# Kernel optimization log

Measured on AMD Instinct MI355X. Metric: run time of the kernel, lower is better.

## Reference

```python
import jax, jax.numpy as jnp
import numpy as np

N = 100000      # nodes
E = 1600000     # directed edges
F_IN = 128      # node feature dim
H = 128         # hidden dim
C = 16          # classes


def setup_inputs() -> dict:
    key = jax.random.key(0)
    ks = jax.random.split(key, 8)
    s = 1.0 / np.sqrt(H)
    return {
        "x": jax.random.normal(ks[0], (N, F_IN), dtype=jnp.float32),
        "edge_index": jax.random.randint(ks[1], (2, E), 0, N, dtype=jnp.int32),
        "W1": jax.random.normal(ks[2], (F_IN, H), dtype=jnp.float32) * s,
        "b1": jnp.zeros((H,), jnp.float32),
        "W2": jax.random.normal(ks[3], (H, H), dtype=jnp.float32) * s,
        "b2": jnp.zeros((H,), jnp.float32),
        "W3": jax.random.normal(ks[4], (H, H), dtype=jnp.float32) * s,
        "b3": jnp.zeros((H,), jnp.float32),
        "Wfc": jax.random.normal(ks[5], (H, C), dtype=jnp.float32) * s,
        "bfc": jnp.zeros((C,), jnp.float32),
    }


def _gcn_conv(x, W, b, src, dst, norm):
    # x' = b + scatter_add over edges of norm * (x @ W)[src] into dst
    h = x @ W                                   # [N, H] dense GEMM
    msg = h[src] * norm[:, None]                # [E+N, H] gather + scale
    out = jax.ops.segment_sum(msg, dst, num_segments=N)  # scatter-add
    return out + b


def reference(x, edge_index, W1, b1, W2, b2, W3, b3, Wfc, bfc):
    loops = jnp.arange(N, dtype=edge_index.dtype)
    src = jnp.concatenate([edge_index[0], loops])   # [E+N] with self-loops
    dst = jnp.concatenate([edge_index[1], loops])
    # symmetric normalization deg^{-1/2}[src] * deg^{-1/2}[dst] (PyG default)
    deg = jax.ops.segment_sum(jnp.ones_like(dst, dtype=x.dtype), dst, num_segments=N)
    dinv = jax.lax.rsqrt(deg)                       # deg >= 1 due to self-loops
    norm = dinv[src] * dinv[dst]

    h = jax.nn.elu(_gcn_conv(x, W1, b1, src, dst, norm))   # dropout is identity in eval
    h = jax.nn.elu(_gcn_conv(h, W2, b2, src, dst, norm))
    h = jax.nn.elu(_gcn_conv(h, W3, b3, src, dst, norm))
    logits = h @ Wfc + bfc                                  # [N, C]
    return jax.nn.log_softmax(logits, axis=-1)
```

## Files before the change

### kernel.cpp

```cpp
#include <hip/hip_runtime.h>
#include <math.h>

#define HDIM 128
#define CDIM 16
#define CAP 48
#define ASTR 136
#define HSTR 132
#define NBINS 256
#define TILE 4096
#define NPBMAX 512
#define SORTCAP 7424

typedef unsigned short u16;
typedef unsigned int u32;
typedef __attribute__((ext_vector_type(8))) short short8;
typedef __attribute__((ext_vector_type(4))) float f32x4;
typedef __attribute__((ext_vector_type(2))) float f32x2;

__device__ inline u16 f2bf(float f) {
  u32 u = __float_as_uint(f);
  u += 0x7fffu + ((u >> 16) & 1u);
  return (u16)(u >> 16);
}
__device__ inline float bf_lo(u32 p) { return __uint_as_float(p << 16); }
__device__ inline float bf_hi(u32 p) { return __uint_as_float(p & 0xffff0000u); }
__device__ inline u32 pack2(float a, float b) {
  return (u32)f2bf(a) | ((u32)f2bf(b) << 16);
}
__device__ inline u32 cvtpk(float a, float b) {
  u32 r;
  asm("v_cvt_pk_bf16_f32 %0, %1, %2" : "=v"(r) : "v"(a), "v"(b));
  return r;
}
__device__ inline void acc_word(f32x2& acc, u32 w) {
  f32x2 x;
  x.x = __uint_as_float(w << 16);
  x.y = __uint_as_float(w & 0xffff0000u);
  asm("v_pk_add_f32 %0, %1, %2" : "=v"(acc) : "v"(x), "v"(acc));
}


__global__ __launch_bounds__(256) void bin_kernel(const int* __restrict__ ei,
                                                  int* __restrict__ cursor,
                                                  int2* __restrict__ bins,
                                                  int binCap, int E, int npb, int nbE,
                                                  int nbW, int N,
                                                  const float* __restrict__ W0,
                                                  const float* __restrict__ W1,
                                                  const float* __restrict__ W2,
                                                  u16* __restrict__ Wt,
                                                  u16* __restrict__ Arow,
                                                  u16* __restrict__ Brow) {
  int tid = threadIdx.x;
  if (blockIdx.x >= nbE) {
    if (blockIdx.x >= nbE + nbW) {
      if (tid < 16) ((uint4*)Arow)[tid] = make_uint4(0, 0, 0, 0);
      else if (tid < 32) ((uint4*)Brow)[tid - 16] = make_uint4(0, 0, 0, 0);
      return;
    }
    int t = (blockIdx.x - nbE) * 256 + tid;
    int which = t >> 14, idx = t & 16383;
    int n = idx >> 7, k = idx & 127;
    const float* W = which == 0 ? W0 : (which == 1 ? W1 : W2);
    Wt[(size_t)which * HDIM * HDIM + n * HDIM + k] = f2bf(W[k * HDIM + n]);
    return;
  }
  __shared__ int2 eds[TILE];
  __shared__ int base[NBINS], rank[NBINS], hist[NBINS];
  int t0 = blockIdx.x * TILE;
  int n = min(TILE, E - t0);
  for (int i = tid; i < NBINS; i += 256) { hist[i] = 0; rank[i] = 0; }
  __syncthreads();
  for (int i = tid; i < n; i += 256) {
    int s = ei[t0 + i];
    int d = ei[E + t0 + i];
    eds[i] = make_int2(d, s);
    atomicAdd(&hist[d / npb], 1);
  }
  __syncthreads();
  for (int i = tid; i < NBINS; i += 256) {
    int h = hist[i];
    base[i] = h ? atomicAdd(&cursor[i], h) : 0;
  }
  __syncthreads();
  for (int i = tid; i < n; i += 256) {
    int2 e = eds[i];
    int b = e.x / npb;
    int r = base[b] + atomicAdd(&rank[b], 1);
    if (r < binCap) bins[(size_t)b * binCap + r] = e;
  }
}

__global__ __launch_bounds__(256) void fill2_kernel(const int2* __restrict__ bins,
                                                    const int* __restrict__ cursor,
                                                    int binCap, int npb,
                                                    int* __restrict__ deg,
                                                    int* __restrict__ csr, int N) {
  __shared__ int hist[NPBMAX];
  __shared__ int base[NPBMAX + 1];
  __shared__ int sorted[SORTCAP];
  int b = blockIdx.x;
  int tid = threadIdx.x;
  int n0 = b * npb;
  int nn = min(npb, N - n0);
  if (nn <= 0) return;
  int cnt = min(min(cursor[b], binCap), SORTCAP);
  const int2* eb = bins + (size_t)b * binCap;
  for (int i = tid; i < nn; i += 256) hist[i] = 0;
  __syncthreads();
  for (int i = tid; i < cnt; i += 256) atomicAdd(&hist[eb[i].x - n0], 1);
  __syncthreads();
  if (tid == 0) {
    int s = 0;
    for (int i = 0; i < nn; ++i) { base[i] = s; s += hist[i]; }
    base[nn] = s;
  }
  __syncthreads();
  for (int i = tid; i < nn; i += 256) hist[i] = 0;
  __syncthreads();
  for (int i = tid; i < cnt; i += 256) {
    int2 e = eb[i];
    int loc = e.x - n0;
    sorted[base[loc] + atomicAdd(&hist[loc], 1)] = e.y;
  }
  __syncthreads();
  for (int i = tid; i < nn; i += 256) deg[n0 + i] = base[i + 1] - base[i];
  int total = nn * CAP;
  int* cout = csr + (size_t)n0 * CAP;
  for (int i = tid; i < total; i += 256) {
    int loc = (int)(((u32)(i >> 4) * 21846u) >> 16);
    int j = i - loc * CAP;
    int s0 = base[loc];
    int dc = min(base[loc + 1] - s0, CAP);
    cout[i] = j < dc ? sorted[s0 + j] : N;
  }
}


template <bool FP32IN>
__global__ __launch_bounds__(256) void gemm_k(const void* __restrict__ Xv,
                                              const u16* __restrict__ Wt,
                                              const int* __restrict__ deg,
                                              u16* __restrict__ G, int N) {
  __shared__ u16 As[64 * ASTR];
  __shared__ u16 Wsm[128 * ASTR];
  int tid = threadIdx.x;
  int row0 = blockIdx.x * 64;

  {
    int r = tid >> 2, c = tid & 3;
    int rg = row0 + r;
    if (rg >= N) rg = N - 1;
    uint4* dst = (uint4*)(As + r * ASTR + c * 32);
    if (FP32IN) {
      const float4* src = (const float4*)((const float*)Xv + (size_t)rg * HDIM + c * 32);
#pragma unroll
      for (int j = 0; j < 4; ++j) {
        float4 a = src[2 * j], b = src[2 * j + 1];
        uint4 o;
        o.x = pack2(a.x, a.y); o.y = pack2(a.z, a.w);
        o.z = pack2(b.x, b.y); o.w = pack2(b.z, b.w);
        dst[j] = o;
      }
    } else {
      const uint4* src = (const uint4*)((const u16*)Xv + (size_t)rg * HDIM + c * 32);
      dst[0] = src[0]; dst[1] = src[1]; dst[2] = src[2]; dst[3] = src[3];
    }
  }
  {
    int r = tid >> 1, h = tid & 1;
    const uint4* src = (const uint4*)(Wt + r * HDIM + h * 64);
    uint4* dst = (uint4*)(Wsm + r * ASTR + h * 64);
#pragma unroll
    for (int i = 0; i < 8; ++i) dst[i] = src[i];
  }
  __syncthreads();

  int w = tid >> 6;
  int l = tid & 63;
  int m = l & 15, q = l >> 4;

  f32x4 acc[8];
#pragma unroll
  for (int i = 0; i < 8; ++i) acc[i] = (f32x4){0.f, 0.f, 0.f, 0.f};

#pragma unroll
  for (int kc = 0; kc < 4; ++kc) {
    short8 af = *(const short8*)(As + (w * 16 + m) * ASTR + kc * 32 + q * 8);
#pragma unroll
    for (int nt = 0; nt < 8; ++nt) {
      short8 bfr = *(const short8*)(Wsm + (nt * 16 + m) * ASTR + kc * 32 + q * 8);
      acc[nt] = __builtin_amdgcn_mfma_f32_16x16x32_bf16(af, bfr, acc[nt], 0, 0, 0);
    }
  }
  __syncthreads();

  float dv[4];
#pragma unroll
  for (int r = 0; r < 4; ++r) {
    int rg = row0 + w * 16 + q * 4 + r;
    dv[r] = rsqrtf((float)(deg[rg < N ? rg : N - 1] + 1));
  }
#pragma unroll
  for (int nt = 0; nt < 8; ++nt)
#pragma unroll
    for (int r = 0; r < 4; ++r)
      As[(w * 16 + q * 4 + r) * ASTR + nt * 16 + m] = f2bf(acc[nt][r] * dv[r]);
  __syncthreads();

  {
    int r = tid >> 2, c = tid & 3;
    int rg = row0 + r;
    if (rg < N) {
      uint4* dst = (uint4*)(G + (size_t)rg * HDIM + c * 32);
      const uint4* src = (const uint4*)(As + r * ASTR + c * 32);
      dst[0] = src[0]; dst[1] = src[1]; dst[2] = src[2]; dst[3] = src[3];
    }
  }
}


__device__ inline void gather16(const u16* __restrict__ G, const int* __restrict__ deg,
                                const int* __restrict__ csr,
                                const float4* __restrict__ b4, int node, int l, float* v) {
  const char* Gb = (const char*)G;
  f32x2 p0, p1, p2, p3;
  {
    uint4 sr = *(const uint4*)(Gb + ((size_t)node << 8) + (l << 4));
    p0.x = bf_lo(sr.x); p0.y = bf_hi(sr.x);
    p1.x = bf_lo(sr.y); p1.y = bf_hi(sr.y);
    p2.x = bf_lo(sr.z); p2.y = bf_hi(sr.z);
    p3.x = bf_lo(sr.w); p3.y = bf_hi(sr.w);
  }
  int dfull = deg[node];
  int d = min(dfull, CAP);
  int dp = (d + 7) & ~7;
  const int* row = csr + (size_t)node * CAP;
  int i0 = row[l];
  int i1 = d > 16 ? row[16 + l] : 0;
  int i2 = d > 32 ? row[32 + l] : 0;

#define GLD(u) (*(const uint4*)(Gb + (((u32)(u)) << 8) + (l << 4)))
#define AW(gv) { acc_word(p0, gv.x); acc_word(p1, gv.y); acc_word(p2, gv.z); acc_word(p3, gv.w); }
  for (int k = 0; k < dp; k += 8) {
    int s = k < 16 ? i0 : (k < 32 ? i1 : i2);
    int bl = k & 15;
    int u0 = __shfl(s, bl + 0, 16), u1 = __shfl(s, bl + 1, 16);
    int u2 = __shfl(s, bl + 2, 16), u3 = __shfl(s, bl + 3, 16);
    int u4 = __shfl(s, bl + 4, 16), u5 = __shfl(s, bl + 5, 16);
    int u6 = __shfl(s, bl + 6, 16), u7 = __shfl(s, bl + 7, 16);
    uint4 g0 = GLD(u0), g1 = GLD(u1), g2 = GLD(u2), g3 = GLD(u3);
    uint4 g4 = GLD(u4), g5 = GLD(u5), g6 = GLD(u6), g7 = GLD(u7);
    AW(g0) AW(g1) AW(g2) AW(g3) AW(g4) AW(g5) AW(g6) AW(g7)
  }
#undef AW
#undef GLD
  float dvn = rsqrtf((float)(dfull + 1));
  float4 b0 = b4[l * 2], b1 = b4[l * 2 + 1];
  v[0] = fmaf(dvn, p0.x, b0.x); v[1] = fmaf(dvn, p0.y, b0.y);
  v[2] = fmaf(dvn, p1.x, b0.z); v[3] = fmaf(dvn, p1.y, b0.w);
  v[4] = fmaf(dvn, p2.x, b1.x); v[5] = fmaf(dvn, p2.y, b1.y);
  v[6] = fmaf(dvn, p3.x, b1.z); v[7] = fmaf(dvn, p3.y, b1.w);
#pragma unroll
  for (int j = 0; j < 8; ++j) v[j] = v[j] > 0.f ? v[j] : __expf(v[j]) - 1.f;
}


__global__ __launch_bounds__(256) void agg_gemm(const u16* __restrict__ G,
                                                const int* __restrict__ deg,
                                                const int* __restrict__ csr,
                                                const float* __restrict__ b,
                                                const u16* __restrict__ Wn,
                                                u16* __restrict__ Gout, int N) {
  __shared__ u16 As[16 * ASTR];
  __shared__ float dvs[16];
  int tid = threadIdx.x;
  int node0 = blockIdx.x * 16;
  int lr = tid >> 4, l = tid & 15;
  int node = node0 + lr;
  if (tid < 16) dvs[tid] = rsqrtf((float)(deg[min(node0 + tid, N - 1)] + 1));
  if (node < N) {
    float v[8];
    gather16(G, deg, csr, (const float4*)b, node, l, v);
    uint4 o;
    o.x = cvtpk(v[0], v[1]); o.y = cvtpk(v[2], v[3]);
    o.z = cvtpk(v[4], v[5]); o.w = cvtpk(v[6], v[7]);
    *(uint4*)(As + lr * ASTR + l * 8) = o;
  } else {
    uint4 z = make_uint4(0, 0, 0, 0);
    *(uint4*)(As + lr * ASTR + l * 8) = z;
  }
  __syncthreads();

  int w = tid >> 6;
  int lw = tid & 63;
  int m = lw & 15, q = lw >> 4;
  f32x4 acc0 = (f32x4){0.f, 0.f, 0.f, 0.f};
  f32x4 acc1 = (f32x4){0.f, 0.f, 0.f, 0.f};
#pragma unroll
  for (int kc = 0; kc < 4; ++kc) {
    short8 af = *(const short8*)(As + m * ASTR + kc * 32 + q * 8);
    short8 b0 = *(const short8*)(Wn + ((w * 2 + 0) * 16 + m) * HDIM + kc * 32 + q * 8);
    short8 b1 = *(const short8*)(Wn + ((w * 2 + 1) * 16 + m) * HDIM + kc * 32 + q * 8);
    acc0 = __builtin_amdgcn_mfma_f32_16x16x32_bf16(af, b0, acc0, 0, 0, 0);
    acc1 = __builtin_amdgcn_mfma_f32_16x16x32_bf16(af, b1, acc1, 0, 0, 0);
  }
  __syncthreads();

#pragma unroll
  for (int r = 0; r < 4; ++r) {
    float dvr = dvs[q * 4 + r];
    As[(q * 4 + r) * ASTR + (w * 2 + 0) * 16 + m] = f2bf(acc0[r] * dvr);
    As[(q * 4 + r) * ASTR + (w * 2 + 1) * 16 + m] = f2bf(acc1[r] * dvr);
  }
  __syncthreads();

  {
    int r = tid >> 4, c = tid & 15;
    if (node0 + r < N)
      *(uint4*)(Gout + (size_t)(node0 + r) * HDIM + c * 8) =
          *(const uint4*)(As + r * ASTR + c * 8);
  }
}


__global__ __launch_bounds__(256) void agg_fc(const u16* __restrict__ G,
                                              const int* __restrict__ deg,
                                              const int* __restrict__ csr,
                                              const float* __restrict__ b,
                                              const float* __restrict__ Wfc,
                                              const float* __restrict__ bfc,
                                              float* __restrict__ out, int N) {
  __shared__ float Hs[16 * HSTR];
  __shared__ float Wl[HDIM * CDIM];
  int tid = threadIdx.x;
  for (int i = tid; i < HDIM * CDIM; i += 256) Wl[i] = Wfc[i];

  int node0 = blockIdx.x * 16;
  int lr = tid >> 4, l = tid & 15;
  int node = node0 + lr;
  if (node < N) {
    float v[8];
    gather16(G, deg, csr, (const float4*)b, node, l, v);
    float4* dst = (float4*)(Hs + lr * HSTR + l * 8);
    dst[0] = make_float4(v[0], v[1], v[2], v[3]);
    dst[1] = make_float4(v[4], v[5], v[6], v[7]);
  }
  __syncthreads();

  int rg = node0 + lr;
  if (rg >= N) return;
  int c = l;
  const float* hrow = Hs + lr * HSTR;
  float acc = bfc[c];
#pragma unroll 4
  for (int k4 = 0; k4 < 32; ++k4) {
    float4 g = *(const float4*)(hrow + k4 * 4);
    const float* wk = Wl + (k4 * 4) * CDIM + c;
    acc = fmaf(g.x, wk[0 * CDIM], acc);
    acc = fmaf(g.y, wk[1 * CDIM], acc);
    acc = fmaf(g.z, wk[2 * CDIM], acc);
    acc = fmaf(g.w, wk[3 * CDIM], acc);
  }
  float mx = acc;
  for (int off = 8; off >= 1; off >>= 1) mx = fmaxf(mx, __shfl_xor(mx, off, 16));
  float ex = __expf(acc - mx);
  float ssum = ex;
  for (int off = 8; off >= 1; off >>= 1) ssum += __shfl_xor(ssum, off, 16);
  out[(size_t)rg * CDIM + c] = (acc - mx) - __logf(ssum);
}


extern "C" void kernel_launch(void* const* d_in, const int* in_sizes, int n_in,
                              void* d_out, int out_size, void* d_ws, size_t ws_size,
                              hipStream_t stream) {
  const float* x   = (const float*)d_in[0];
  const int*   ei  = (const int*)d_in[1];
  const float* W1  = (const float*)d_in[2];
  const float* b1  = (const float*)d_in[3];
  const float* W2  = (const float*)d_in[4];
  const float* b2  = (const float*)d_in[5];
  const float* W3  = (const float*)d_in[6];
  const float* b3  = (const float*)d_in[7];
  const float* Wfc = (const float*)d_in[8];
  const float* bfc = (const float*)d_in[9];

  const int N = in_sizes[0] / HDIM;
  const int E = in_sizes[1] / 2;
  const int npb = (N + NBINS - 1) / NBINS;
  const int binCap = (E + NBINS - 1) / NBINS + 1024;
  const int nbE = (E + TILE - 1) / TILE;
  const int nbW = 3 * HDIM * HDIM / 256;

  char* ws = (char*)d_ws;
  size_t off = 0;
  auto alloc = [&](size_t bytes) -> void* {
    void* p = ws + off;
    off += (bytes + 511) & ~(size_t)511;
    return p;
  };
  int*   deg    = (int*)alloc((size_t)N * 4);
  int*   cursor = (int*)alloc((size_t)NBINS * 4);
  int*   csr    = (int*)alloc((size_t)N * CAP * 4);
  int2*  bins   = (int2*)alloc((size_t)NBINS * binCap * 8);
  u16*   Wt     = (u16*)alloc((size_t)3 * HDIM * HDIM * 2);
  u16*   A      = (u16*)alloc((size_t)(N + 1) * HDIM * 2);
  u16*   B      = (u16*)alloc((size_t)(N + 1) * HDIM * 2);

  hipMemsetAsync(cursor, 0, (size_t)NBINS * 4, stream);
  bin_kernel<<<nbE + nbW + 1, 256, 0, stream>>>(ei, cursor, bins, binCap, E, npb, nbE, nbW,
                                                N, W1, W2, W3, Wt,
                                                A + (size_t)N * HDIM, B + (size_t)N * HDIM);
  fill2_kernel<<<NBINS, 256, 0, stream>>>(bins, cursor, binCap, npb, deg, csr, N);

  int grid64 = (N + 63) / 64;
  int grid16 = (N + 15) / 16;
  gemm_k<true><<<grid64, 256, 0, stream>>>(x, Wt, deg, A, N);
  agg_gemm<<<grid16, 256, 0, stream>>>(A, deg, csr, b1, Wt + HDIM * HDIM, B, N);
  agg_gemm<<<grid16, 256, 0, stream>>>(B, deg, csr, b2, Wt + 2 * HDIM * HDIM, A, N);
  agg_fc<<<grid16, 256, 0, stream>>>(A, deg, csr, b3, Wfc, bfc, (float*)d_out, N);
}
```

Before: 365.9 us.

## Pack binned edges into 32-bit words and locally sort before scatter

Edges are packed into one 32-bit word (local destination offset in the high bits, 17-bit source in the low bits), which halves the bin buffer traffic between binning and CSR fill. The bin kernel now also counting-sorts each tile by bin in shared memory, using a prefix scan, and writes the sorted run out contiguously. Each thread finds its bin with a binary search, so global stores become coalesced per bin instead of scattered. The packing assumes N < 2^17 and per-bin node offsets under 2^15, and it adds shared memory use and extra barriers in bin_kernel.

```diff
diff --git a/kernel.cpp b/kernel.cpp
--- a/kernel.cpp
+++ b/kernel.cpp
@@ -42,7 +42,7 @@
 
 __global__ __launch_bounds__(256) void bin_kernel(const int* __restrict__ ei,
                                                   int* __restrict__ cursor,
-                                                  int2* __restrict__ bins,
+                                                  u32* __restrict__ bins,
                                                   int binCap, int E, int npb, int nbE,
                                                   int nbW, int N,
                                                   const float* __restrict__ W0,
@@ -65,33 +65,59 @@
     Wt[(size_t)which * HDIM * HDIM + n * HDIM + k] = f2bf(W[k * HDIM + n]);
     return;
   }
-  __shared__ int2 eds[TILE];
-  __shared__ int base[NBINS], rank[NBINS], hist[NBINS];
+  __shared__ u32 eds32[TILE];
+  __shared__ u32 srt[TILE];
+  __shared__ unsigned char bid[TILE];
+  __shared__ int hist[NBINS], lbase[NBINS + 1], gbase[NBINS], rnk[NBINS];
   int t0 = blockIdx.x * TILE;
   int n = min(TILE, E - t0);
-  for (int i = tid; i < NBINS; i += 256) { hist[i] = 0; rank[i] = 0; }
+  hist[tid] = 0;
+  rnk[tid] = 0;
   __syncthreads();
   for (int i = tid; i < n; i += 256) {
     int s = ei[t0 + i];
     int d = ei[E + t0 + i];
-    eds[i] = make_int2(d, s);
-    atomicAdd(&hist[d / npb], 1);
-  }
-  __syncthreads();
-  for (int i = tid; i < NBINS; i += 256) {
-    int h = hist[i];
-    base[i] = h ? atomicAdd(&cursor[i], h) : 0;
-  }
+    int b = d / npb;
+    eds32[i] = ((u32)(d - b * npb) << 17) | (u32)s;
+    bid[i] = (unsigned char)b;
+    atomicAdd(&hist[b], 1);
+  }
+  __syncthreads();
+  int h = hist[tid];
+  lbase[tid] = h;
+  __syncthreads();
+#pragma unroll
+  for (int off = 1; off < 256; off <<= 1) {
+    int v = tid >= off ? lbase[tid - off] : 0;
+    __syncthreads();
+    lbase[tid] += v;
+    __syncthreads();
+  }
+  int ex = lbase[tid] - h;
+  __syncthreads();
+  lbase[tid] = ex;
+  if (tid == 255) lbase[256] = ex + h;
+  gbase[tid] = h ? atomicAdd(&cursor[tid], h) : 0;
   __syncthreads();
   for (int i = tid; i < n; i += 256) {
-    int2 e = eds[i];
-    int b = e.x / npb;
-    int r = base[b] + atomicAdd(&rank[b], 1);
-    if (r < binCap) bins[(size_t)b * binCap + r] = e;
-  }
-}
-
-__global__ __launch_bounds__(256) void fill2_kernel(const int2* __restrict__ bins,
+    int b = bid[i];
+    int r = lbase[b] + atomicAdd(&rnk[b], 1);
+    srt[r] = eds32[i];
+  }
+  __syncthreads();
+  for (int i = tid; i < n; i += 256) {
+    int lo = 0, hi = 255;
+#pragma unroll
+    for (int k = 0; k < 8; ++k) {
+      int mid = (lo + hi + 1) >> 1;
+      if (lbase[mid] <= i) lo = mid; else hi = mid - 1;
+    }
+    int r = gbase[lo] + (i - lbase[lo]);
+    if (r < binCap) bins[(size_t)lo * binCap + r] = srt[i];
+  }
+}
+
+__global__ __launch_bounds__(256) void fill2_kernel(const u32* __restrict__ bins,
                                                     const int* __restrict__ cursor,
                                                     int binCap, int npb,
                                                     int* __restrict__ deg,
@@ -105,10 +131,10 @@
   int nn = min(npb, N - n0);
   if (nn <= 0) return;
   int cnt = min(min(cursor[b], binCap), SORTCAP);
-  const int2* eb = bins + (size_t)b * binCap;
+  const u32* eb = bins + (size_t)b * binCap;
   for (int i = tid; i < nn; i += 256) hist[i] = 0;
   __syncthreads();
-  for (int i = tid; i < cnt; i += 256) atomicAdd(&hist[eb[i].x - n0], 1);
+  for (int i = tid; i < cnt; i += 256) atomicAdd(&hist[eb[i] >> 17], 1);
   __syncthreads();
   if (tid == 0) {
     int s = 0;
@@ -119,9 +145,9 @@
   for (int i = tid; i < nn; i += 256) hist[i] = 0;
   __syncthreads();
   for (int i = tid; i < cnt; i += 256) {
-    int2 e = eb[i];
-    int loc = e.x - n0;
-    sorted[base[loc] + atomicAdd(&hist[loc], 1)] = e.y;
+    u32 w = eb[i];
+    int loc = w >> 17;
+    sorted[base[loc] + atomicAdd(&hist[loc], 1)] = (int)(w & 0x1FFFFu);
   }
   __syncthreads();
   for (int i = tid; i < nn; i += 256) deg[n0 + i] = base[i + 1] - base[i];
@@ -402,7 +428,7 @@
   int*   deg    = (int*)alloc((size_t)N * 4);
   int*   cursor = (int*)alloc((size_t)NBINS * 4);
   int*   csr    = (int*)alloc((size_t)N * CAP * 4);
-  int2*  bins   = (int2*)alloc((size_t)NBINS * binCap * 8);
+  u32*   bins   = (u32*)alloc((size_t)NBINS * binCap * 4);
   u16*   Wt     = (u16*)alloc((size_t)3 * HDIM * HDIM * 2);
   u16*   A      = (u16*)alloc((size_t)(N + 1) * HDIM * 2);
   u16*   B      = (u16*)alloc((size_t)(N + 1) * HDIM * 2);
```

Measured after the change: 369.8 us. No clear change (+1.1%).
